# Kernel optimization log

Hardware: AMD Instinct MI355X
Metric: run time of the kernel (lower is better)

The kernel has to match this reference:

```python
import jax, jax.numpy as jnp
import numpy as np

DIM = 1024
H = 16
DH = DIM // H
THETA = 10000.0


def _rotary_cos_sin(dtype):
    # Faithful to original: rotary is called on q with shape (B, H, 1, DH) and
    # seq_dim=1, so "positions" are t = arange(num_heads).
    inv_freq = 1.0 / (THETA ** (jnp.arange(0, DH, 2, dtype=jnp.float32) / DH))
    t = jnp.arange(H, dtype=jnp.float32)
    freqs = t[:, None] * inv_freq[None, :]          # (H, DH/2)
    emb = jnp.concatenate([freqs, freqs], axis=-1)   # (H, DH)
    cos = jnp.cos(emb)[None, :, None, :].astype(dtype)  # (1, H, 1, DH)
    sin = jnp.sin(emb)[None, :, None, :].astype(dtype)
    return cos, sin


def _rotate_half(x):
    x1, x2 = x[..., : DH // 2], x[..., DH // 2 :]
    return jnp.concatenate([-x2, x1], axis=-1)


def setup_inputs() -> dict:
    key = jax.random.key(0)
    ks = jax.random.split(key, 6)
    B, N = 16, 4096
    s = 1.0 / np.sqrt(DIM)
    return {
        "x": jax.random.normal(ks[0], (B, N, DIM), dtype=jnp.float32),
        "Wq": jax.random.normal(ks[1], (DIM, DIM), dtype=jnp.float32) * s,
        "Wk": jax.random.normal(ks[2], (DIM, DIM), dtype=jnp.float32) * s,
        "Wv": jax.random.normal(ks[3], (DIM, DIM), dtype=jnp.float32) * s,
        "Wp": jax.random.normal(ks[4], (DIM, DIM), dtype=jnp.float32) * s,
        "bp": jax.random.normal(ks[5], (DIM,), dtype=jnp.float32) * 0.01,
    }


def reference(x, Wq, Wk, Wv, Wp, bp):
    B, N, C = x.shape
    scale = DH ** -0.5
    # projections (weights stored as (in, out); x @ W)
    q = (x[:, :1, :] @ Wq).reshape(B, 1, H, DH).transpose(0, 2, 1, 3)  # (B,H,1,DH)
    k = (x @ Wk).reshape(B, N, H, DH).transpose(0, 2, 1, 3)            # (B,H,N,DH)
    v = (x @ Wv).reshape(B, N, H, DH).transpose(0, 2, 1, 3)            # (B,H,N,DH)
    cos, sin = _rotary_cos_sin(x.dtype)
    q = q * cos + _rotate_half(q) * sin
    k = k * cos + _rotate_half(k) * sin  # broadcasts over N (per original)
    attn = jnp.einsum("bhqd,bhkd->bhqk", q, k) * scale  # (B,H,1,N)
    attn = jax.nn.softmax(attn, axis=-1)
    out = jnp.einsum("bhqk,bhkd->bhqd", attn, v)        # (B,H,1,DH)
    out = out.transpose(0, 2, 1, 3).reshape(B, 1, C)
    return out @ Wp + bp
```

## Files before the change

### kernel.cpp

```cpp
#include <hip/hip_runtime.h>

#define NB 16
#define SEQ 4096
#define DIMC 1024
#define NH 16
#define DH 64
#define NCL 128
#define RPL 32

#define OFF_Q      0
#define OFF_WTIL   16384
#define OFF_LOGITS 278528
#define OFF_P      1327104
#define OFF_PMAX   2375680
#define OFF_M      2408448
#define OFF_LPART  2408704
#define OFF_HO     2425088
#define OFF_Y      2441472

__global__ __launch_bounds__(256) void kq(const float* __restrict__ x,
                                          const float* __restrict__ Wq,
                                          float* __restrict__ qws) {
  const int jc = blockIdx.x, b = blockIdx.y, t = threadIdx.x;
  const int d = t & 63, g = t >> 6;
  const int j = jc * 64 + d;
  const float* x0 = x + (size_t)b * SEQ * DIMC;
  __shared__ float red[256];
  float a = 0.f;
  #pragma unroll 8
  for (int c = g * 256; c < g * 256 + 256; ++c)
    a = fmaf(x0[c], Wq[(size_t)c * DIMC + j], a);
  red[t] = a;
  __syncthreads();
  if (t < 64)
    qws[b * DIMC + jc * 64 + t] = red[t] + red[64 + t] + red[128 + t] + red[192 + t];
}

__global__ __launch_bounds__(256) void kw(const float* __restrict__ Wk,
                                          const float* __restrict__ qws,
                                          float* __restrict__ wtil) {
  const int cs = blockIdx.x, h = blockIdx.y, b = blockIdx.z, t = threadIdx.x;
  const int v = t >> 6, dd = t & 63;
  const float qd = qws[b * DIMC + h * DH + dd];
  float* wt = wtil + ((size_t)b * NH + h) * DIMC;
  const int c0 = cs * 256 + v * 64;
  for (int c = c0; c < c0 + 64; ++c) {
    float p = Wk[(size_t)c * DIMC + h * DH + dd] * qd;
    #pragma unroll
    for (int o = 1; o < 64; o <<= 1) p += __shfl_xor(p, o);
    if (dd == 0) wt[c] = p * 0.125f;
  }
}

__device__ __forceinline__ float dot16(const float4* xv, const float4* wv) {
  float s = 0.f;
  #pragma unroll
  for (int i = 0; i < 4; ++i) {
    s = fmaf(xv[i].x, wv[i].x, s); s = fmaf(xv[i].y, wv[i].y, s);
    s = fmaf(xv[i].z, wv[i].z, s); s = fmaf(xv[i].w, wv[i].w, s);
  }
  return s;
}

__global__ __launch_bounds__(256) void k_logit(const float* __restrict__ x,
                                               const float* __restrict__ wtil,
                                               float* __restrict__ logits,
                                               float* __restrict__ pmax) {
  const int nc = blockIdx.x, b = blockIdx.y, t = threadIdx.x;
  const int w = t >> 6, l = t & 63;
  const float4* wt4 = (const float4*)wtil + ((size_t)b * NH + w * 4) * 256;
  float4 wv[4][4];
  #pragma unroll
  for (int h = 0; h < 4; ++h)
    #pragma unroll
    for (int i = 0; i < 4; ++i) wv[h][i] = wt4[h * 256 + i * 64 + l];
  const float4* x4 = (const float4*)x + ((size_t)b * SEQ + nc * RPL) * 256;
  float* lg = logits + ((size_t)b * SEQ + (size_t)nc * RPL) * NH + w * 4;
  float4 vm = make_float4(-3.0e38f, -3.0e38f, -3.0e38f, -3.0e38f);

  for (int r = 0; r < RPL; r += 2) {
    float4 xa[4], xb[4];
    #pragma unroll
    for (int i = 0; i < 4; ++i) xa[i] = x4[r * 256 + i * 64 + l];
    #pragma unroll
    for (int i = 0; i < 4; ++i) xb[i] = x4[(r + 1) * 256 + i * 64 + l];
    float4 sa, sb;
    sa.x = dot16(xa, wv[0]); sa.y = dot16(xa, wv[1]);
    sa.z = dot16(xa, wv[2]); sa.w = dot16(xa, wv[3]);
    sb.x = dot16(xb, wv[0]); sb.y = dot16(xb, wv[1]);
    sb.z = dot16(xb, wv[2]); sb.w = dot16(xb, wv[3]);
    #pragma unroll
    for (int o = 1; o < 64; o <<= 1) {
      sa.x += __shfl_xor(sa.x, o); sa.y += __shfl_xor(sa.y, o);
      sa.z += __shfl_xor(sa.z, o); sa.w += __shfl_xor(sa.w, o);
      sb.x += __shfl_xor(sb.x, o); sb.y += __shfl_xor(sb.y, o);
      sb.z += __shfl_xor(sb.z, o); sb.w += __shfl_xor(sb.w, o);
    }
    vm.x = fmaxf(vm.x, fmaxf(sa.x, sb.x)); vm.y = fmaxf(vm.y, fmaxf(sa.y, sb.y));
    vm.z = fmaxf(vm.z, fmaxf(sa.z, sb.z)); vm.w = fmaxf(vm.w, fmaxf(sa.w, sb.w));
    if (l < 4) {
      float va = (l == 0) ? sa.x : (l == 1) ? sa.y : (l == 2) ? sa.z : sa.w;
      float vb = (l == 0) ? sb.x : (l == 1) ? sb.y : (l == 2) ? sb.z : sb.w;
      lg[r * NH + l] = va;
      lg[(r + 1) * NH + l] = vb;
    }
  }
  if (l < 4) {
    float vsel = (l == 0) ? vm.x : (l == 1) ? vm.y : (l == 2) ? vm.z : vm.w;
    pmax[((size_t)b * NCL + nc) * NH + w * 4 + l] = vsel;
  }
}

__global__ __launch_bounds__(256) void k_m(const float* __restrict__ pmax,
                                           float* __restrict__ m,
                                           float* __restrict__ ho) {
  const int t = threadIdx.x;
  const int b = t >> 4, h = t & 15;
  float v = -3.0e38f;
  #pragma unroll 16
  for (int nc = 0; nc < NCL; ++nc) v = fmaxf(v, pmax[((size_t)b * NCL + nc) * NH + h]);
  m[t] = v;
  for (int i = t; i < NB * DIMC; i += 256) ho[i] = 0.f;
}

__global__ __launch_bounds__(256) void k_p(const float* __restrict__ logits,
                                           const float* __restrict__ m,
                                           float* __restrict__ p) {
  const int f4 = blockIdx.x * 256 + threadIdx.x;
  const int b = f4 >> 14;
  const float4 m4 = ((const float4*)m)[b * 4 + (f4 & 3)];
  float4 g = ((const float4*)logits)[f4];
  float4 e;
  e.x = __expf(g.x - m4.x); e.y = __expf(g.y - m4.y);
  e.z = __expf(g.z - m4.z); e.w = __expf(g.w - m4.w);
  ((float4*)p)[f4] = e;
}

__global__ __launch_bounds__(256) void k_acc(const float* __restrict__ x,
                                             const float* __restrict__ p,
                                             float* __restrict__ y,
                                             float* __restrict__ Lpart,
                                             int rpc) {
  const int nc = blockIdx.x, b = blockIdx.y, t = threadIdx.x;
  float4 acc[16];
  #pragma unroll
  for (int h = 0; h < 16; ++h) acc[h] = make_float4(0.f, 0.f, 0.f, 0.f);
  float4 L0 = make_float4(0, 0, 0, 0), L1 = L0, L2 = L0, L3 = L0;
  const float4* x4 = (const float4*)x + ((size_t)b * SEQ + (size_t)nc * rpc) * 256;
  const float4* p4 = (const float4*)(p + ((size_t)b * SEQ + (size_t)nc * rpc) * NH);

  for (int r = 0; r < rpc; r += 2) {
    float4 a0 = p4[r * 4 + 0], a1 = p4[r * 4 + 1], a2 = p4[r * 4 + 2], a3 = p4[r * 4 + 3];
    float4 b0 = p4[r * 4 + 4], b1 = p4[r * 4 + 5], b2 = p4[r * 4 + 6], b3 = p4[r * 4 + 7];
    float4 xva = x4[r * 256 + t];
    float4 xvb = x4[(r + 1) * 256 + t];
    #define ACC(h, ev, xv) acc[h].x = fmaf(ev, xv.x, acc[h].x); acc[h].y = fmaf(ev, xv.y, acc[h].y); \
                           acc[h].z = fmaf(ev, xv.z, acc[h].z); acc[h].w = fmaf(ev, xv.w, acc[h].w)
    ACC(0, a0.x, xva); ACC(1, a0.y, xva); ACC(2, a0.z, xva); ACC(3, a0.w, xva);
    ACC(4, a1.x, xva); ACC(5, a1.y, xva); ACC(6, a1.z, xva); ACC(7, a1.w, xva);
    ACC(8, a2.x, xva); ACC(9, a2.y, xva); ACC(10, a2.z, xva); ACC(11, a2.w, xva);
    ACC(12, a3.x, xva); ACC(13, a3.y, xva); ACC(14, a3.z, xva); ACC(15, a3.w, xva);
    ACC(0, b0.x, xvb); ACC(1, b0.y, xvb); ACC(2, b0.z, xvb); ACC(3, b0.w, xvb);
    ACC(4, b1.x, xvb); ACC(5, b1.y, xvb); ACC(6, b1.z, xvb); ACC(7, b1.w, xvb);
    ACC(8, b2.x, xvb); ACC(9, b2.y, xvb); ACC(10, b2.z, xvb); ACC(11, b2.w, xvb);
    ACC(12, b3.x, xvb); ACC(13, b3.y, xvb); ACC(14, b3.z, xvb); ACC(15, b3.w, xvb);
    #undef ACC
    if (t < 64) {
      L0.x += a0.x + b0.x; L0.y += a0.y + b0.y; L0.z += a0.z + b0.z; L0.w += a0.w + b0.w;
      L1.x += a1.x + b1.x; L1.y += a1.y + b1.y; L1.z += a1.z + b1.z; L1.w += a1.w + b1.w;
      L2.x += a2.x + b2.x; L2.y += a2.y + b2.y; L2.z += a2.z + b2.z; L2.w += a2.w + b2.w;
      L3.x += a3.x + b3.x; L3.y += a3.y + b3.y; L3.z += a3.z + b3.z; L3.w += a3.w + b3.w;
    }
  }
  float4* y4 = (float4*)y + (((size_t)b * gridDim.x + nc) * NH) * 256;
  #pragma unroll
  for (int h = 0; h < 16; ++h) y4[h * 256 + t] = acc[h];
  if (t == 0) {
    float* Lp = Lpart + ((size_t)b * gridDim.x + nc) * NH;
    Lp[0] = L0.x; Lp[1] = L0.y; Lp[2] = L0.z; Lp[3] = L0.w;
    Lp[4] = L1.x; Lp[5] = L1.y; Lp[6] = L1.z; Lp[7] = L1.w;
    Lp[8] = L2.x; Lp[9] = L2.y; Lp[10] = L2.z; Lp[11] = L2.w;
    Lp[12] = L3.x; Lp[13] = L3.y; Lp[14] = L3.z; Lp[15] = L3.w;
  }
}

__global__ __launch_bounds__(256) void k_comb(const float* __restrict__ y,
                                              const float* __restrict__ Lpart,
                                              const float* __restrict__ Wv,
                                              float* __restrict__ ho,
                                              int nch) {
  const int cs = blockIdx.x, h = blockIdx.y, b = blockIdx.z, t = threadIdx.x;
  __shared__ float ylds[256];
  __shared__ float red[256];
  __shared__ float sInvL;
  if (t < 64) {
    float lp = (t < nch) ? Lpart[((size_t)b * nch + t) * NH + h] : 0.f;
    #pragma unroll
    for (int o = 1; o < 64; o <<= 1) lp += __shfl_xor(lp, o);
    if (t == 0) sInvL = 1.f / lp;
  }
  const int c = cs * 256 + t;
  float ysum = 0.f;
  for (int s = 0; s < nch; ++s)
    ysum += y[(((size_t)b * nch + s) * NH + h) * DIMC + c];
  __syncthreads();
  ylds[t] = ysum * sInvL;
  __syncthreads();
  const int d = t & 63, g = t >> 6;
  float part = 0.f;
  #pragma unroll 4
  for (int k = 0; k < 64; ++k)
    part = fmaf(ylds[g * 64 + k], Wv[(size_t)(cs * 256 + g * 64 + k) * DIMC + h * DH + d], part);
  red[t] = part;
  __syncthreads();
  if (t < 64)
    atomicAdd(&ho[(size_t)b * DIMC + h * DH + t],
              red[t] + red[64 + t] + red[128 + t] + red[192 + t]);
}

__global__ __launch_bounds__(256) void k_out(const float* __restrict__ ho,
                                             const float* __restrict__ Wp,
                                             const float* __restrict__ bp,
                                             float* __restrict__ out) {
  const int jc = blockIdx.x, b = blockIdx.y, t = threadIdx.x;
  __shared__ float hs[1024];
  __shared__ float red[256];
  for (int i = t; i < 1024; i += 256) hs[i] = ho[(size_t)b * DIMC + i];
  __syncthreads();
  const int d = t & 63, g = t >> 6;
  const int j = jc * 64 + d;
  float a = 0.f;
  #pragma unroll 8
  for (int i = g * 256; i < g * 256 + 256; ++i)
    a = fmaf(hs[i], Wp[(size_t)i * DIMC + j], a);
  red[t] = a;
  __syncthreads();
  if (t < 64)
    out[(size_t)b * DIMC + jc * 64 + t] =
        red[t] + red[64 + t] + red[128 + t] + red[192 + t] + bp[jc * 64 + t];
}

extern "C" void kernel_launch(void* const* d_in, const int* in_sizes, int n_in,
                              void* d_out, int out_size, void* d_ws, size_t ws_size,
                              hipStream_t stream) {
  const float* x  = (const float*)d_in[0];
  const float* Wq = (const float*)d_in[1];
  const float* Wk = (const float*)d_in[2];
  const float* Wv = (const float*)d_in[3];
  const float* Wp = (const float*)d_in[4];
  const float* bp = (const float*)d_in[5];
  float* out = (float*)d_out;
  float* ws = (float*)d_ws;

  float* qws    = ws + OFF_Q;
  float* wtil   = ws + OFF_WTIL;
  float* logits = ws + OFF_LOGITS;
  float* p      = ws + OFF_P;
  float* pmax   = ws + OFF_PMAX;
  float* m      = ws + OFF_M;
  float* Lpart  = ws + OFF_LPART;
  float* ho     = ws + OFF_HO;
  float* y      = ws + OFF_Y;

  const int ncAcc = (ws_size >= (size_t)19218688 * 4) ? 64 : 32;
  const int rpc = SEQ / ncAcc;

  kq<<<dim3(16, NB), 256, 0, stream>>>(x, Wq, qws);
  kw<<<dim3(4, NH, NB), 256, 0, stream>>>(Wk, qws, wtil);
  k_logit<<<dim3(NCL, NB), 256, 0, stream>>>(x, wtil, logits, pmax);
  k_m<<<1, 256, 0, stream>>>(pmax, m, ho);
  k_p<<<1024, 256, 0, stream>>>(logits, m, p);
  k_acc<<<dim3(ncAcc, NB), 256, 0, stream>>>(x, p, y, Lpart, rpc);
  k_comb<<<dim3(4, NH, NB), 256, 0, stream>>>(y, Lpart, Wv, ho, ncAcc);
  k_out<<<dim3(16, NB), 256, 0, stream>>>(ho, Wp, bp, out);
}
```

Before: 609.1 us.

## Fuse per-chunk softmax into logit kernel and merge q/wtil prep kernels

Computes chunk-local max and exp-sums inside the logit kernel and writes unnormalized probabilities directly. The separate logits buffer and the exp pass are gone, and a global rescale factor per chunk is folded into the combine step. The q projection and Wk contraction are merged into one kernel, so there are fewer launches and less intermediate traffic. The cost is fewer logit blocks (64 rows each) and a less parallel prep kernel with a longer serial loop per block.

```diff
diff --git a/kernel.cpp b/kernel.cpp
--- a/kernel.cpp
+++ b/kernel.cpp
@@ -5,47 +5,40 @@
 #define DIMC 1024
 #define NH 16
 #define DH 64
-#define NCL 128
-#define RPL 32
-
-#define OFF_Q      0
-#define OFF_WTIL   16384
-#define OFF_LOGITS 278528
-#define OFF_P      1327104
-#define OFF_PMAX   2375680
-#define OFF_M      2408448
-#define OFF_LPART  2408704
-#define OFF_HO     2425088
-#define OFF_Y      2441472
-
-__global__ __launch_bounds__(256) void kq(const float* __restrict__ x,
-                                          const float* __restrict__ Wq,
-                                          float* __restrict__ qws) {
-  const int jc = blockIdx.x, b = blockIdx.y, t = threadIdx.x;
-  const int d = t & 63, g = t >> 6;
-  const int j = jc * 64 + d;
+#define NC 64
+#define RPC 64
+
+#define OFF_WTIL  0
+#define OFF_P     262144
+#define OFF_PMAX  1310720
+#define OFF_LC    1327104
+#define OFF_SCALE 1343488
+#define OFF_HO    1359872
+#define OFF_Y     1376256
+
+__global__ __launch_bounds__(256) void k_prep(const float* __restrict__ x,
+                                              const float* __restrict__ Wq,
+                                              const float* __restrict__ Wk,
+                                              float* __restrict__ wtil) {
+  const int h = blockIdx.x, b = blockIdx.y, t = threadIdx.x;
+  const int dd = t & 63, g = t >> 6;
   const float* x0 = x + (size_t)b * SEQ * DIMC;
   __shared__ float red[256];
+  __shared__ float qs[64];
   float a = 0.f;
-  #pragma unroll 8
+  const float* wq = Wq + h * DH + dd;
+  #pragma unroll 4
   for (int c = g * 256; c < g * 256 + 256; ++c)
-    a = fmaf(x0[c], Wq[(size_t)c * DIMC + j], a);
+    a = fmaf(x0[c], wq[(size_t)c * DIMC], a);
   red[t] = a;
   __syncthreads();
-  if (t < 64)
-    qws[b * DIMC + jc * 64 + t] = red[t] + red[64 + t] + red[128 + t] + red[192 + t];
-}
-
-__global__ __launch_bounds__(256) void kw(const float* __restrict__ Wk,
-                                          const float* __restrict__ qws,
-                                          float* __restrict__ wtil) {
-  const int cs = blockIdx.x, h = blockIdx.y, b = blockIdx.z, t = threadIdx.x;
-  const int v = t >> 6, dd = t & 63;
-  const float qd = qws[b * DIMC + h * DH + dd];
+  if (t < 64) qs[t] = red[t] + red[64 + t] + red[128 + t] + red[192 + t];
+  __syncthreads();
+  const float qd = qs[dd];
   float* wt = wtil + ((size_t)b * NH + h) * DIMC;
-  const int c0 = cs * 256 + v * 64;
-  for (int c = c0; c < c0 + 64; ++c) {
-    float p = Wk[(size_t)c * DIMC + h * DH + dd] * qd;
+  const float* wk = Wk + h * DH + dd;
+  for (int c = g * 256; c < g * 256 + 256; ++c) {
+    float p = wk[(size_t)c * DIMC] * qd;
     #pragma unroll
     for (int o = 1; o < 64; o <<= 1) p += __shfl_xor(p, o);
     if (dd == 0) wt[c] = p * 0.125f;
@@ -64,8 +57,9 @@
 
 __global__ __launch_bounds__(256) void k_logit(const float* __restrict__ x,
                                                const float* __restrict__ wtil,
-                                               float* __restrict__ logits,
-                                               float* __restrict__ pmax) {
+                                               float* __restrict__ p,
+                                               float* __restrict__ pmax,
+                                               float* __restrict__ Lc) {
   const int nc = blockIdx.x, b = blockIdx.y, t = threadIdx.x;
   const int w = t >> 6, l = t & 63;
   const float4* wt4 = (const float4*)wtil + ((size_t)b * NH + w * 4) * 256;
@@ -74,11 +68,10 @@
   for (int h = 0; h < 4; ++h)
     #pragma unroll
     for (int i = 0; i < 4; ++i) wv[h][i] = wt4[h * 256 + i * 64 + l];
-  const float4* x4 = (const float4*)x + ((size_t)b * SEQ + nc * RPL) * 256;
-  float* lg = logits + ((size_t)b * SEQ + (size_t)nc * RPL) * NH + w * 4;
-  float4 vm = make_float4(-3.0e38f, -3.0e38f, -3.0e38f, -3.0e38f);
-
-  for (int r = 0; r < RPL; r += 2) {
+  const float4* x4 = (const float4*)x + ((size_t)b * SEQ + nc * RPC) * 256;
+  float4 va = make_float4(0.f, 0.f, 0.f, 0.f);
+
+  for (int r = 0; r < RPC; r += 2) {
     float4 xa[4], xb[4];
     #pragma unroll
     for (int i = 0; i < 4; ++i) xa[i] = x4[r * 256 + i * 64 + l];
@@ -96,60 +89,65 @@
       sb.x += __shfl_xor(sb.x, o); sb.y += __shfl_xor(sb.y, o);
       sb.z += __shfl_xor(sb.z, o); sb.w += __shfl_xor(sb.w, o);
     }
-    vm.x = fmaxf(vm.x, fmaxf(sa.x, sb.x)); vm.y = fmaxf(vm.y, fmaxf(sa.y, sb.y));
-    vm.z = fmaxf(vm.z, fmaxf(sa.z, sb.z)); vm.w = fmaxf(vm.w, fmaxf(sa.w, sb.w));
-    if (l < 4) {
-      float va = (l == 0) ? sa.x : (l == 1) ? sa.y : (l == 2) ? sa.z : sa.w;
-      float vb = (l == 0) ? sb.x : (l == 1) ? sb.y : (l == 2) ? sb.z : sb.w;
-      lg[r * NH + l] = va;
-      lg[(r + 1) * NH + l] = vb;
-    }
-  }
-  if (l < 4) {
-    float vsel = (l == 0) ? vm.x : (l == 1) ? vm.y : (l == 2) ? vm.z : vm.w;
-    pmax[((size_t)b * NCL + nc) * NH + w * 4 + l] = vsel;
+    if (l == r) va = sa;
+    if (l == r + 1) va = sb;
+  }
+
+  float4 m4 = va;
+  #pragma unroll
+  for (int o = 1; o < 64; o <<= 1) {
+    m4.x = fmaxf(m4.x, __shfl_xor(m4.x, o)); m4.y = fmaxf(m4.y, __shfl_xor(m4.y, o));
+    m4.z = fmaxf(m4.z, __shfl_xor(m4.z, o)); m4.w = fmaxf(m4.w, __shfl_xor(m4.w, o));
+  }
+  float4 pv;
+  pv.x = __expf(va.x - m4.x); pv.y = __expf(va.y - m4.y);
+  pv.z = __expf(va.z - m4.z); pv.w = __expf(va.w - m4.w);
+  float4 s4 = pv;
+  #pragma unroll
+  for (int o = 1; o < 64; o <<= 1) {
+    s4.x += __shfl_xor(s4.x, o); s4.y += __shfl_xor(s4.y, o);
+    s4.z += __shfl_xor(s4.z, o); s4.w += __shfl_xor(s4.w, o);
+  }
+  ((float4*)(p + ((size_t)b * SEQ + (size_t)nc * RPC + l) * NH))[w] = pv;
+  if (l == 0) {
+    ((float4*)(pmax + ((size_t)b * NC + nc) * NH))[w] = m4;
+    ((float4*)(Lc + ((size_t)b * NC + nc) * NH))[w] = s4;
   }
 }
 
 __global__ __launch_bounds__(256) void k_m(const float* __restrict__ pmax,
-                                           float* __restrict__ m,
+                                           const float* __restrict__ Lc,
+                                           float* __restrict__ scale,
                                            float* __restrict__ ho) {
   const int t = threadIdx.x;
   const int b = t >> 4, h = t & 15;
-  float v = -3.0e38f;
-  #pragma unroll 16
-  for (int nc = 0; nc < NCL; ++nc) v = fmaxf(v, pmax[((size_t)b * NCL + nc) * NH + h]);
-  m[t] = v;
+  float M = -3.0e38f;
+  #pragma unroll 8
+  for (int nc = 0; nc < NC; ++nc)
+    M = fmaxf(M, pmax[((size_t)b * NC + nc) * NH + h]);
+  float L = 0.f;
+  #pragma unroll 8
+  for (int nc = 0; nc < NC; ++nc)
+    L += Lc[((size_t)b * NC + nc) * NH + h] * __expf(pmax[((size_t)b * NC + nc) * NH + h] - M);
+  const float invL = 1.f / L;
+  #pragma unroll 8
+  for (int nc = 0; nc < NC; ++nc)
+    scale[((size_t)b * NC + nc) * NH + h] =
+        __expf(pmax[((size_t)b * NC + nc) * NH + h] - M) * invL;
   for (int i = t; i < NB * DIMC; i += 256) ho[i] = 0.f;
-}
-
-__global__ __launch_bounds__(256) void k_p(const float* __restrict__ logits,
-                                           const float* __restrict__ m,
-                                           float* __restrict__ p) {
-  const int f4 = blockIdx.x * 256 + threadIdx.x;
-  const int b = f4 >> 14;
-  const float4 m4 = ((const float4*)m)[b * 4 + (f4 & 3)];
-  float4 g = ((const float4*)logits)[f4];
-  float4 e;
-  e.x = __expf(g.x - m4.x); e.y = __expf(g.y - m4.y);
-  e.z = __expf(g.z - m4.z); e.w = __expf(g.w - m4.w);
-  ((float4*)p)[f4] = e;
 }
 
 __global__ __launch_bounds__(256) void k_acc(const float* __restrict__ x,
                                              const float* __restrict__ p,
-                                             float* __restrict__ y,
-                                             float* __restrict__ Lpart,
-                                             int rpc) {
+                                             float* __restrict__ y) {
   const int nc = blockIdx.x, b = blockIdx.y, t = threadIdx.x;
   float4 acc[16];
   #pragma unroll
   for (int h = 0; h < 16; ++h) acc[h] = make_float4(0.f, 0.f, 0.f, 0.f);
-  float4 L0 = make_float4(0, 0, 0, 0), L1 = L0, L2 = L0, L3 = L0;
-  const float4* x4 = (const float4*)x + ((size_t)b * SEQ + (size_t)nc * rpc) * 256;
-  const float4* p4 = (const float4*)(p + ((size_t)b * SEQ + (size_t)nc * rpc) * NH);
-
-  for (int r = 0; r < rpc; r += 2) {
+  const float4* x4 = (const float4*)x + ((size_t)b * SEQ + (size_t)nc * RPC) * 256;
+  const float4* p4 = (const float4*)(p + ((size_t)b * SEQ + (size_t)nc * RPC) * NH);
+
+  for (int r = 0; r < RPC; r += 2) {
     float4 a0 = p4[r * 4 + 0], a1 = p4[r * 4 + 1], a2 = p4[r * 4 + 2], a3 = p4[r * 4 + 3];
     float4 b0 = p4[r * 4 + 4], b1 = p4[r * 4 + 5], b2 = p4[r * 4 + 6], b3 = p4[r * 4 + 7];
     float4 xva = x4[r * 256 + t];
@@ -165,52 +163,33 @@
     ACC(8, b2.x, xvb); ACC(9, b2.y, xvb); ACC(10, b2.z, xvb); ACC(11, b2.w, xvb);
     ACC(12, b3.x, xvb); ACC(13, b3.y, xvb); ACC(14, b3.z, xvb); ACC(15, b3.w, xvb);
     #undef ACC
-    if (t < 64) {
-      L0.x += a0.x + b0.x; L0.y += a0.y + b0.y; L0.z += a0.z + b0.z; L0.w += a0.w + b0.w;
-      L1.x += a1.x + b1.x; L1.y += a1.y + b1.y; L1.z += a1.z + b1.z; L1.w += a1.w + b1.w;
-      L2.x += a2.x + b2.x; L2.y += a2.y + b2.y; L2.z += a2.z + b2.z; L2.w += a2.w + b2.w;
-      L3.x += a3.x + b3.x; L3.y += a3.y + b3.y; L3.z += a3.z + b3.z; L3.w += a3.w + b3.w;
-    }
-  }
-  float4* y4 = (float4*)y + (((size_t)b * gridDim.x + nc) * NH) * 256;
+  }
+  float4* y4 = (float4*)y + (((size_t)b * NC + nc) * NH) * 256;
   #pragma unroll
   for (int h = 0; h < 16; ++h) y4[h * 256 + t] = acc[h];
-  if (t == 0) {
-    float* Lp = Lpart + ((size_t)b * gridDim.x + nc) * NH;
-    Lp[0] = L0.x; Lp[1] = L0.y; Lp[2] = L0.z; Lp[3] = L0.w;
-    Lp[4] = L1.x; Lp[5] = L1.y; Lp[6] = L1.z; Lp[7] = L1.w;
-    Lp[8] = L2.x; Lp[9] = L2.y; Lp[10] = L2.z; Lp[11] = L2.w;
-    Lp[12] = L3.x; Lp[13] = L3.y; Lp[14] = L3.z; Lp[15] = L3.w;
-  }
 }
 
 __global__ __launch_bounds__(256) void k_comb(const float* __restrict__ y,
-                                              const float* __restrict__ Lpart,
+                                              const float* __restrict__ scale,
                                               const float* __restrict__ Wv,
-                                              float* __restrict__ ho,
-                                              int nch) {
+                                              float* __restrict__ ho) {
   const int cs = blockIdx.x, h = blockIdx.y, b = blockIdx.z, t = threadIdx.x;
   __shared__ float ylds[256];
   __shared__ float red[256];
-  __shared__ float sInvL;
-  if (t < 64) {
-    float lp = (t < nch) ? Lpart[((size_t)b * nch + t) * NH + h] : 0.f;
-    #pragma unroll
-    for (int o = 1; o < 64; o <<= 1) lp += __shfl_xor(lp, o);
-    if (t == 0) sInvL = 1.f / lp;
-  }
   const int c = cs * 256 + t;
   float ysum = 0.f;
-  for (int s = 0; s < nch; ++s)
-    ysum += y[(((size_t)b * nch + s) * NH + h) * DIMC + c];
-  __syncthreads();
-  ylds[t] = ysum * sInvL;
+  #pragma unroll 4
+  for (int s = 0; s < NC; ++s)
+    ysum = fmaf(y[(((size_t)b * NC + s) * NH + h) * DIMC + c],
+                scale[((size_t)b * NC + s) * NH + h], ysum);
+  ylds[t] = ysum;
   __syncthreads();
   const int d = t & 63, g = t >> 6;
   float part = 0.f;
   #pragma unroll 4
   for (int k = 0; k < 64; ++k)
-    part = fmaf(ylds[g * 64 + k], Wv[(size_t)(cs * 256 + g * 64 + k) * DIMC + h * DH + d], part);
+    part = fmaf(ylds[g * 64 + k],
+                Wv[(size_t)(cs * 256 + g * 64 + k) * DIMC + h * DH + d], part);
   red[t] = part;
   __syncthreads();
   if (t < 64)
@@ -252,25 +231,18 @@
   float* out = (float*)d_out;
   float* ws = (float*)d_ws;
 
-  float* qws    = ws + OFF_Q;
-  float* wtil   = ws + OFF_WTIL;
-  float* logits = ws + OFF_LOGITS;
-  float* p      = ws + OFF_P;
-  float* pmax   = ws + OFF_PMAX;
-  float* m      = ws + OFF_M;
-  float* Lpart  = ws + OFF_LPART;
-  float* ho     = ws + OFF_HO;
-  float* y      = ws + OFF_Y;
-
-  const int ncAcc = (ws_size >= (size_t)19218688 * 4) ? 64 : 32;
-  const int rpc = SEQ / ncAcc;
-
-  kq<<<dim3(16, NB), 256, 0, stream>>>(x, Wq, qws);
-  kw<<<dim3(4, NH, NB), 256, 0, stream>>>(Wk, qws, wtil);
-  k_logit<<<dim3(NCL, NB), 256, 0, stream>>>(x, wtil, logits, pmax);
-  k_m<<<1, 256, 0, stream>>>(pmax, m, ho);
-  k_p<<<1024, 256, 0, stream>>>(logits, m, p);
-  k_acc<<<dim3(ncAcc, NB), 256, 0, stream>>>(x, p, y, Lpart, rpc);
-  k_comb<<<dim3(4, NH, NB), 256, 0, stream>>>(y, Lpart, Wv, ho, ncAcc);
+  float* wtil  = ws + OFF_WTIL;
+  float* p     = ws + OFF_P;
+  float* pmax  = ws + OFF_PMAX;
+  float* Lc    = ws + OFF_LC;
+  float* scale = ws + OFF_SCALE;
+  float* ho    = ws + OFF_HO;
+  float* y     = ws + OFF_Y;
+
+  k_prep<<<dim3(NH, NB), 256, 0, stream>>>(x, Wq, Wk, wtil);
+  k_logit<<<dim3(NC, NB), 256, 0, stream>>>(x, wtil, p, pmax, Lc);
+  k_m<<<1, 256, 0, stream>>>(pmax, Lc, scale, ho);
+  k_acc<<<dim3(NC, NB), 256, 0, stream>>>(x, p, y);
+  k_comb<<<dim3(4, NH, NB), 256, 0, stream>>>(y, scale, Wv, ho);
   k_out<<<dim3(16, NB), 256, 0, stream>>>(ho, Wp, bp, out);
 }
```

New measurement: 674.4 us. 10.7% more time.
